# Performance work log

Measured on AMD Instinct MI355X. Metric: run time of the kernel, lower is better.

Reference implementation:

```python
import jax, jax.numpy as jnp
import numpy as np

N = 12000       # nodes (Hi-C bins, max_num_nodes)
F_IN = 16       # number_genomic_annotations
HID = 4 * F_IN  # conv1 out = 64
NCLUST = 100    # n_clust
E = 384000      # edges (avg degree 32)


def setup_inputs() -> dict:
    key = jax.random.key(0)
    ks = jax.random.split(key, 8)
    x = jax.random.normal(ks[0], (N, F_IN), dtype=jnp.float32)
    edge_index = jax.random.randint(ks[1], (2, E), 0, N)
    edge_attr = jax.random.uniform(ks[2], (E,), dtype=jnp.float32)
    s1 = 1.0 / np.sqrt(F_IN)
    W1_rel = jax.random.uniform(ks[3], (HID, F_IN), minval=-s1, maxval=s1, dtype=jnp.float32)
    W1_root = jax.random.uniform(ks[4], (HID, F_IN), minval=-s1, maxval=s1, dtype=jnp.float32)
    b1 = jnp.zeros((HID,), jnp.float32)
    s2 = 1.0 / np.sqrt(HID)
    W2_rel = jax.random.uniform(ks[5], (NCLUST, HID), minval=-s2, maxval=s2, dtype=jnp.float32)
    W2_root = jax.random.uniform(ks[6], (NCLUST, HID), minval=-s2, maxval=s2, dtype=jnp.float32)
    b2 = jnp.zeros((NCLUST,), jnp.float32)
    return dict(x=x, edge_index=edge_index, edge_attr=edge_attr,
                W1_rel=W1_rel, W1_root=W1_root, b1=b1,
                W2_rel=W2_rel, W2_root=W2_root, b2=b2)


def _graph_conv(x, src, dst, ew, W_rel, W_root, b):
    # PyG GraphConv (aggr='add'): out = lin_rel(sum_j e_ji * x_j) + lin_root(x)
    msg = x[src] * ew[:, None]                       # [E, F]
    aggr = jax.ops.segment_sum(msg, dst, num_segments=N)  # [N, F]
    return aggr @ W_rel.T + b + x @ W_root.T


def reference(x, edge_index, edge_attr, W1_rel, W1_root, b1, W2_rel, W2_root, b2):
    src, dst = edge_index[0], edge_index[1]
    h = _graph_conv(x, src, dst, edge_attr, W1_rel, W1_root, b1)
    h = jax.nn.relu(h)  # dropout is identity in eval mode
    s_out = _graph_conv(h, src, dst, edge_attr, W2_rel, W2_root, b2)  # [N, NCLUST]

    # to_dense_adj (duplicate edges summed)
    adj = jnp.zeros((N, N), x.dtype).at[src, dst].add(edge_attr)  # [N, N]

    # dense_mincut_pool with S = x (as in the original forward), k = F_IN
    s_mc = jax.nn.softmax(x, axis=-1)      # [N, F_IN]
    as_ = adj @ s_mc                        # [N, F_IN]
    out_adj = s_mc.T @ as_                  # [F_IN, F_IN]
    mincut_num = jnp.trace(out_adj)
    d_flat = adj.sum(-1)                    # [N] degree
    mincut_den = jnp.einsum('ik,i,ik->', s_mc, d_flat, s_mc)  # trace(S^T D S)
    mc = -(mincut_num / mincut_den)

    ss = s_mc.T @ s_mc                      # [F_IN, F_IN]
    i_k = jnp.eye(F_IN, dtype=ss.dtype)
    o = jnp.linalg.norm(ss / jnp.linalg.norm(ss) - i_k / jnp.linalg.norm(i_k))

    return jax.nn.softmax(s_out, axis=-1), mc, o
```

## Files before the change

kernel.cpp:

```cpp
#include <hip/hip_runtime.h>
#include <math.h>

#define N_NODES 12000
#define F_INN 16
#define HIDD 64
#define NCLUST 100
#define NEDGE 384000
#define NBLK_N 47
#define CAP 96
#define EPT 4
#define NBLK_E 375
#define NBLK_F1 (N_NODES / 4)
#define NBLK_F2 (N_NODES / 8)

#define OFF_COUNT   0
#define OFF_SCAL    12000
#define ZERO_ELEMS  12002
#define OFF_SSPART  12004
#define OFF_NORM2   24036
#define OFF_W2TREL  36036
#define OFF_W2TROOT 42436
#define OFF_SMC     48836
#define OFF_H       240836
#define OFF_SRCW    1008836

__global__ void pre_kernel(const float* __restrict__ x, float* __restrict__ smc,
                           float* __restrict__ norm2, const float* __restrict__ W2_rel,
                           const float* __restrict__ W2_root, float* __restrict__ w2t_rel,
                           float* __restrict__ w2t_root) {
    __shared__ float fl[6400];
    int t = threadIdx.x;
    int b = blockIdx.x;
    if (b < NBLK_N) {
        int i = b * 256 + t;
        if (i >= N_NODES) return;
        const float4* xr = (const float4*)(x + i * 16);
        float4 r0 = xr[0], r1 = xr[1], r2 = xr[2], r3 = xr[3];
        float v[16] = {r0.x, r0.y, r0.z, r0.w, r1.x, r1.y, r1.z, r1.w,
                       r2.x, r2.y, r2.z, r2.w, r3.x, r3.y, r3.z, r3.w};
        float m = v[0];
#pragma unroll
        for (int k = 1; k < 16; ++k) m = fmaxf(m, v[k]);
        float s = 0.f;
#pragma unroll
        for (int k = 0; k < 16; ++k) { v[k] = __expf(v[k] - m); s += v[k]; }
        float inv = 1.f / s;
        float n2 = 0.f;
#pragma unroll
        for (int k = 0; k < 16; ++k) { v[k] *= inv; n2 += v[k] * v[k]; }
        float4* so = (float4*)(smc + i * 16);
        so[0] = make_float4(v[0], v[1], v[2], v[3]);
        so[1] = make_float4(v[4], v[5], v[6], v[7]);
        so[2] = make_float4(v[8], v[9], v[10], v[11]);
        so[3] = make_float4(v[12], v[13], v[14], v[15]);
        norm2[i] = n2;
    } else {
        const float* src = (b == NBLK_N) ? W2_rel : W2_root;
        float* dst = (b == NBLK_N) ? w2t_rel : w2t_root;
        for (int i = t; i < 6400; i += 256) fl[i] = src[i];
        __syncthreads();
        for (int j = t; j < 6400; j += 256) {
            int kk = j / 100, cl = j - kk * 100;
            dst[j] = fl[cl * 64 + kk];
        }
    }
}

__global__ void scatter_kernel(const int* __restrict__ ei, const float* __restrict__ ew,
                               int* __restrict__ count, int2* __restrict__ srcw,
                               const float* __restrict__ smc, float* __restrict__ sspart,
                               const float* __restrict__ norm2, float* __restrict__ scal) {
    __shared__ float shm[4352];
    int t = threadIdx.x;
    int b = blockIdx.x;
    if (b < NBLK_E) {
        int tid = b * 256 + t;
        int e0 = tid * EPT;
        int4 sv = *(const int4*)(ei + e0);
        int4 dv = *(const int4*)(ei + NEDGE + e0);
        float4 wv = *(const float4*)(ew + e0);
        int s[EPT] = {sv.x, sv.y, sv.z, sv.w};
        int d[EPT] = {dv.x, dv.y, dv.z, dv.w};
        float w[EPT] = {wv.x, wv.y, wv.z, wv.w};
        int pos[EPT];
#pragma unroll
        for (int i = 0; i < EPT; ++i) pos[i] = atomicAdd(&count[d[i]], 1);
#pragma unroll
        for (int i = 0; i < EPT; ++i)
            srcw[d[i] * CAP + pos[i]] = make_int2(s[i], __float_as_int(w[i]));
    } else if (b < NBLK_E + NBLK_N) {
        int bb = b - NBLK_E;
        float* rows = shm;
        int n = bb * 256 + t;
        float* rp = rows + t * 17;
        if (n < N_NODES) {
            const float4* sr = (const float4*)(smc + n * 16);
            float4 a0 = sr[0], a1 = sr[1], a2v = sr[2], a3 = sr[3];
            rp[0] = a0.x;  rp[1] = a0.y;  rp[2] = a0.z;  rp[3] = a0.w;
            rp[4] = a1.x;  rp[5] = a1.y;  rp[6] = a1.z;  rp[7] = a1.w;
            rp[8] = a2v.x; rp[9] = a2v.y; rp[10] = a2v.z; rp[11] = a2v.w;
            rp[12] = a3.x; rp[13] = a3.y; rp[14] = a3.z; rp[15] = a3.w;
        } else {
#pragma unroll
            for (int k = 0; k < 16; ++k) rp[k] = 0.f;
        }
        __syncthreads();
        int a = t & 15, bq = t >> 4;
        float accs = 0.f;
#pragma unroll 4
        for (int r = 0; r < 256; ++r)
            accs = fmaf(rows[r * 17 + a], rows[r * 17 + bq], accs);
        sspart[bb * 256 + t] = accs;
    } else {
        int tid = (b - NBLK_E - NBLK_N) * 256 + t;
        int e0 = tid * EPT;
        int4 sv = *(const int4*)(ei + e0);
        int4 dv = *(const int4*)(ei + NEDGE + e0);
        float4 wv = *(const float4*)(ew + e0);
        int s[EPT] = {sv.x, sv.y, sv.z, sv.w};
        int d[EPT] = {dv.x, dv.y, dv.z, dv.w};
        float w[EPT] = {wv.x, wv.y, wv.z, wv.w};
        float np = 0.f, dp = 0.f;
#pragma unroll
        for (int i = 0; i < EPT; ++i) {
            const float4* ps = (const float4*)(smc + s[i] * 16);
            const float4* pd = (const float4*)(smc + d[i] * 16);
            float4 s0 = ps[0], s1 = ps[1], s2 = ps[2], s3 = ps[3];
            float4 d0 = pd[0], d1 = pd[1], d2 = pd[2], d3 = pd[3];
            float dot = s0.x * d0.x + s0.y * d0.y + s0.z * d0.z + s0.w * d0.w +
                        s1.x * d1.x + s1.y * d1.y + s1.z * d1.z + s1.w * d1.w +
                        s2.x * d2.x + s2.y * d2.y + s2.z * d2.z + s2.w * d2.w +
                        s3.x * d3.x + s3.y * d3.y + s3.z * d3.z + s3.w * d3.w;
            np = fmaf(w[i], dot, np);
            dp = fmaf(w[i], norm2[s[i]], dp);
        }
        float* redn = shm;
        float* redd = shm + 256;
        redn[t] = np;
        redd[t] = dp;
        __syncthreads();
        for (int s2 = 128; s2 > 0; s2 >>= 1) {
            if (t < s2) { redn[t] += redn[t + s2]; redd[t] += redd[t + s2]; }
            __syncthreads();
        }
        if (t == 0) {
            atomicAdd(&scal[0], redn[0]);
            atomicAdd(&scal[1], redd[0]);
        }
    }
}

__global__ void fused1_kernel(const float* __restrict__ x, const int2* __restrict__ srcw,
                              const int* __restrict__ count, const float* __restrict__ W1_rel,
                              const float* __restrict__ W1_root, const float* __restrict__ b1,
                              float* __restrict__ h) {
    __shared__ float shm[2304];
    int t = threadIdx.x;
    int b = blockIdx.x;
    float* wrelT  = shm;
    float* wrootT = shm + 1024;
    float* b1s    = shm + 2048;
    float* aggr   = shm + 2112;
    float* xs     = shm + 2176;
    for (int idx = t; idx < 1024; idx += 256) {
        int f = idx >> 4, k = idx & 15;
        wrelT[(k << 6) + f]  = W1_rel[idx];
        wrootT[(k << 6) + f] = W1_root[idx];
    }
    if (t < 64) b1s[t] = b1[t];
    int w = t >> 6, lane = t & 63;
    int j2 = lane >> 2;
    int q  = lane & 3;
    int n = b * 4 + w;
    int len = count[n];
    const int2* bucket = srcw + n * CAP;
    float4 acc4 = make_float4(0.f, 0.f, 0.f, 0.f);
    for (int k = 0; k < len; k += 32) {
        int ia = k + j2, ib = k + 16 + j2;
        int2 pa = bucket[ia];
        int2 pb = bucket[ib];
        if (ia >= len) pa = make_int2(0, 0);
        if (ib >= len) pb = make_int2(0, 0);
        float4 va = *(const float4*)(x + pa.x * 16 + q * 4);
        float4 vb = *(const float4*)(x + pb.x * 16 + q * 4);
        float wa = __int_as_float(pa.y), wb = __int_as_float(pb.y);
        acc4.x = fmaf(va.x, wa, acc4.x); acc4.y = fmaf(va.y, wa, acc4.y);
        acc4.z = fmaf(va.z, wa, acc4.z); acc4.w = fmaf(va.w, wa, acc4.w);
        acc4.x = fmaf(vb.x, wb, acc4.x); acc4.y = fmaf(vb.y, wb, acc4.y);
        acc4.z = fmaf(vb.z, wb, acc4.z); acc4.w = fmaf(vb.w, wb, acc4.w);
    }
    acc4.x += __shfl_xor(acc4.x, 4);  acc4.y += __shfl_xor(acc4.y, 4);
    acc4.z += __shfl_xor(acc4.z, 4);  acc4.w += __shfl_xor(acc4.w, 4);
    acc4.x += __shfl_xor(acc4.x, 8);  acc4.y += __shfl_xor(acc4.y, 8);
    acc4.z += __shfl_xor(acc4.z, 8);  acc4.w += __shfl_xor(acc4.w, 8);
    acc4.x += __shfl_xor(acc4.x, 16); acc4.y += __shfl_xor(acc4.y, 16);
    acc4.z += __shfl_xor(acc4.z, 16); acc4.w += __shfl_xor(acc4.w, 16);
    acc4.x += __shfl_xor(acc4.x, 32); acc4.y += __shfl_xor(acc4.y, 32);
    acc4.z += __shfl_xor(acc4.z, 32); acc4.w += __shfl_xor(acc4.w, 32);
    if (j2 == 0) *(float4*)(aggr + w * 16 + q * 4) = acc4;
    if (lane < 16) xs[w * 16 + lane] = x[n * 16 + lane];
    __syncthreads();
    float o = b1s[lane];
#pragma unroll
    for (int kk = 0; kk < 16; ++kk)
        o = fmaf(aggr[w * 16 + kk], wrelT[(kk << 6) + lane],
                 fmaf(xs[w * 16 + kk], wrootT[(kk << 6) + lane], o));
    h[n * 64 + lane] = fmaxf(o, 0.f);
}

__global__ __launch_bounds__(512) void fused2_finalize_kernel(
    const float* __restrict__ h, const int2* __restrict__ srcw, const int* __restrict__ count,
    const float* __restrict__ w2t_rel, const float* __restrict__ w2t_root,
    const float* __restrict__ b2, float* __restrict__ out, const float* __restrict__ sspart,
    const float* __restrict__ scal) {
    __shared__ float wsrel[6400];
    __shared__ float a2[8][64], hrow[8][64];
    __shared__ float logits[8][104];
    __shared__ float b2s[104];
    int t = threadIdx.x;
    int b = blockIdx.x;
    if (b < NBLK_F2) {
        for (int i = t; i < 6400; i += 512) wsrel[i] = w2t_rel[i];
        if (t < NCLUST) b2s[t] = b2[t];
        int nn = t >> 6;
        int c = t & 63;
        int eslot = c >> 4;
        int q = c & 15;
        int n = b * 8 + nn;
        int len = count[n];
        const int2* bucket = srcw + n * CAP;
        float4 acc4 = make_float4(0.f, 0.f, 0.f, 0.f);
        for (int k = 0; k < len; k += 32) {
            int i0 = k + eslot,      i1 = k + 4 + eslot;
            int i2 = k + 8 + eslot,  i3 = k + 12 + eslot;
            int i4 = k + 16 + eslot, i5 = k + 20 + eslot;
            int i6 = k + 24 + eslot, i7 = k + 28 + eslot;
            int2 pa = bucket[i0]; int2 pb = bucket[i1];
            int2 pc = bucket[i2]; int2 pd = bucket[i3];
            int2 pe = bucket[i4]; int2 pf = bucket[i5];
            int2 pg = bucket[i6]; int2 ph = bucket[i7];
            if (i0 >= len) pa = make_int2(0, 0);
            if (i1 >= len) pb = make_int2(0, 0);
            if (i2 >= len) pc = make_int2(0, 0);
            if (i3 >= len) pd = make_int2(0, 0);
            if (i4 >= len) pe = make_int2(0, 0);
            if (i5 >= len) pf = make_int2(0, 0);
            if (i6 >= len) pg = make_int2(0, 0);
            if (i7 >= len) ph = make_int2(0, 0);
            float4 va = *(const float4*)(h + pa.x * 64 + q * 4);
            float4 vb = *(const float4*)(h + pb.x * 64 + q * 4);
            float4 vc = *(const float4*)(h + pc.x * 64 + q * 4);
            float4 vd = *(const float4*)(h + pd.x * 64 + q * 4);
            float4 ve = *(const float4*)(h + pe.x * 64 + q * 4);
            float4 vf = *(const float4*)(h + pf.x * 64 + q * 4);
            float4 vg = *(const float4*)(h + pg.x * 64 + q * 4);
            float4 vh = *(const float4*)(h + ph.x * 64 + q * 4);
            float wa = __int_as_float(pa.y), wb = __int_as_float(pb.y);
            float wc = __int_as_float(pc.y), wd = __int_as_float(pd.y);
            float we = __int_as_float(pe.y), wf = __int_as_float(pf.y);
            float wg = __int_as_float(pg.y), wh = __int_as_float(ph.y);
            acc4.x = fmaf(va.x, wa, acc4.x); acc4.y = fmaf(va.y, wa, acc4.y);
            acc4.z = fmaf(va.z, wa, acc4.z); acc4.w = fmaf(va.w, wa, acc4.w);
            acc4.x = fmaf(vb.x, wb, acc4.x); acc4.y = fmaf(vb.y, wb, acc4.y);
            acc4.z = fmaf(vb.z, wb, acc4.z); acc4.w = fmaf(vb.w, wb, acc4.w);
            acc4.x = fmaf(vc.x, wc, acc4.x); acc4.y = fmaf(vc.y, wc, acc4.y);
            acc4.z = fmaf(vc.z, wc, acc4.z); acc4.w = fmaf(vc.w, wc, acc4.w);
            acc4.x = fmaf(vd.x, wd, acc4.x); acc4.y = fmaf(vd.y, wd, acc4.y);
            acc4.z = fmaf(vd.z, wd, acc4.z); acc4.w = fmaf(vd.w, wd, acc4.w);
            acc4.x = fmaf(ve.x, we, acc4.x); acc4.y = fmaf(ve.y, we, acc4.y);
            acc4.z = fmaf(ve.z, we, acc4.z); acc4.w = fmaf(ve.w, we, acc4.w);
            acc4.x = fmaf(vf.x, wf, acc4.x); acc4.y = fmaf(vf.y, wf, acc4.y);
            acc4.z = fmaf(vf.z, wf, acc4.z); acc4.w = fmaf(vf.w, wf, acc4.w);
            acc4.x = fmaf(vg.x, wg, acc4.x); acc4.y = fmaf(vg.y, wg, acc4.y);
            acc4.z = fmaf(vg.z, wg, acc4.z); acc4.w = fmaf(vg.w, wg, acc4.w);
            acc4.x = fmaf(vh.x, wh, acc4.x); acc4.y = fmaf(vh.y, wh, acc4.y);
            acc4.z = fmaf(vh.z, wh, acc4.z); acc4.w = fmaf(vh.w, wh, acc4.w);
        }
        acc4.x += __shfl_xor(acc4.x, 16); acc4.y += __shfl_xor(acc4.y, 16);
        acc4.z += __shfl_xor(acc4.z, 16); acc4.w += __shfl_xor(acc4.w, 16);
        acc4.x += __shfl_xor(acc4.x, 32); acc4.y += __shfl_xor(acc4.y, 32);
        acc4.z += __shfl_xor(acc4.z, 32); acc4.w += __shfl_xor(acc4.w, 32);
        if (eslot == 0) *(float4*)(&a2[nn][q * 4]) = acc4;
        hrow[nn][c] = h[n * 64 + c];
        __syncthreads();
        int g = t >> 7, c2 = t & 127;
        if (c2 < NCLUST) {
            int na = 2 * g, nb2 = 2 * g + 1;
            float s0 = b2s[c2], s1 = s0;
#pragma unroll 8
            for (int kk = 0; kk < 64; ++kk) {
                float wr = wsrel[kk * 100 + c2];
                float wo = w2t_root[kk * 100 + c2];
                s0 = fmaf(a2[na][kk], wr, fmaf(hrow[na][kk], wo, s0));
                s1 = fmaf(a2[nb2][kk], wr, fmaf(hrow[nb2][kk], wo, s1));
            }
            logits[na][c2] = s0;
            logits[nb2][c2] = s1;
        }
        __syncthreads();
        float v0 = logits[nn][c];
        float v1 = (c < NCLUST - 64) ? logits[nn][64 + c] : -INFINITY;
        float m = fmaxf(v0, v1);
#pragma unroll
        for (int off = 32; off > 0; off >>= 1) m = fmaxf(m, __shfl_xor(m, off));
        float e0 = __expf(v0 - m);
        float e1 = (c < NCLUST - 64) ? __expf(v1 - m) : 0.f;
        float s = e0 + e1;
#pragma unroll
        for (int off = 32; off > 0; off >>= 1) s += __shfl_xor(s, off);
        float inv = 1.f / s;
        out[n * NCLUST + c] = e0 * inv;
        if (c < NCLUST - 64) out[n * NCLUST + 64 + c] = e1 * inv;
    } else {
        float* red = wsrel;
        float sv = 0.f;
        if (t < 256)
            for (int bb = 0; bb < NBLK_N; ++bb) sv += sspart[bb * 256 + t];
        red[t] = sv * sv;
        __syncthreads();
        for (int s = 256; s > 0; s >>= 1) {
            if (t < s) red[t] += red[t + s];
            __syncthreads();
        }
        float ssnorm = sqrtf(red[0]);
        __syncthreads();
        float diff = (t < 256) ? (sv / ssnorm - ((t % 17 == 0) ? 0.25f : 0.f)) : 0.f;
        red[t] = diff * diff;
        __syncthreads();
        for (int s = 256; s > 0; s >>= 1) {
            if (t < s) red[t] += red[t + s];
            __syncthreads();
        }
        if (t == 0) {
            out[N_NODES * NCLUST + 0] = -(scal[0] / scal[1]);
            out[N_NODES * NCLUST + 1] = sqrtf(red[0]);
        }
    }
}

extern "C" void kernel_launch(void* const* d_in, const int* in_sizes, int n_in,
                              void* d_out, int out_size, void* d_ws, size_t ws_size,
                              hipStream_t stream) {
    const float* x       = (const float*)d_in[0];
    const int*   ei      = (const int*)d_in[1];
    const float* ew      = (const float*)d_in[2];
    const float* W1_rel  = (const float*)d_in[3];
    const float* W1_root = (const float*)d_in[4];
    const float* b1      = (const float*)d_in[5];
    const float* W2_rel  = (const float*)d_in[6];
    const float* W2_root = (const float*)d_in[7];
    const float* b2      = (const float*)d_in[8];
    float* out = (float*)d_out;
    int*   wsi = (int*)d_ws;

    int*   count   = wsi + OFF_COUNT;
    float* scal    = (float*)(wsi + OFF_SCAL);
    float* sspart  = (float*)(wsi + OFF_SSPART);
    float* norm2   = (float*)(wsi + OFF_NORM2);
    float* w2trel  = (float*)(wsi + OFF_W2TREL);
    float* w2troot = (float*)(wsi + OFF_W2TROOT);
    float* smc     = (float*)(wsi + OFF_SMC);
    float* h       = (float*)(wsi + OFF_H);
    int2*  srcw    = (int2*)(wsi + OFF_SRCW);

    hipMemsetAsync(wsi, 0, ZERO_ELEMS * sizeof(int), stream);
    pre_kernel<<<NBLK_N + 2, 256, 0, stream>>>(x, smc, norm2, W2_rel, W2_root, w2trel, w2troot);
    scatter_kernel<<<NBLK_E + NBLK_N + NBLK_E, 256, 0, stream>>>(ei, ew, count, srcw,
                                                                 smc, sspart, norm2, scal);
    fused1_kernel<<<NBLK_F1, 256, 0, stream>>>(x, srcw, count, W1_rel, W1_root, b1, h);
    fused2_finalize_kernel<<<NBLK_F2 + 1, 512, 0, stream>>>(h, srcw, count, w2trel, w2troot,
                                                            b2, out, sspart, scal);
}
```

Measured before the change: 99.37 us.

## Replace global atomic edge scatter with two-pass binned bucketing via shared memory

Edges are first grouped into 188 coarse destination bins of 64 nodes. Each block stages records in shared memory and issues one global atomic per bin, spilling to global when a bin overflows its local slot. A second kernel then builds per-node CSR-like buckets in shared memory for each bin and writes them out coalesced. This replaces per-edge global atomics and scattered writes to count/srcw, at the cost of an extra pass over a bin buffer, fixed capacity limits (BCAP, CAP) that drop edges silently if exceeded, and a large shared-memory footprint that reduces occupancy.

```diff
diff --git a/kernel.cpp b/kernel.cpp
--- a/kernel.cpp
+++ b/kernel.cpp
@@ -13,26 +13,70 @@
 #define NBLK_F1 (N_NODES / 4)
 #define NBLK_F2 (N_NODES / 8)
 
-#define OFF_COUNT   0
-#define OFF_SCAL    12000
-#define ZERO_ELEMS  12002
-#define OFF_SSPART  12004
-#define OFF_NORM2   24036
-#define OFF_W2TREL  36036
-#define OFF_W2TROOT 42436
-#define OFF_SMC     48836
-#define OFF_H       240836
-#define OFF_SRCW    1008836
-
-__global__ void pre_kernel(const float* __restrict__ x, float* __restrict__ smc,
-                           float* __restrict__ norm2, const float* __restrict__ W2_rel,
-                           const float* __restrict__ W2_root, float* __restrict__ w2t_rel,
-                           float* __restrict__ w2t_root) {
-    __shared__ float fl[6400];
+#define NBIN 188
+#define BINW 64
+#define BCAP 2560
+#define STCAP 24
+
+#define OFF_BINCNT  0
+#define OFF_SCAL    188
+#define ZERO_ELEMS  190
+#define OFF_COUNT   192
+#define OFF_SSPART  12192
+#define OFF_NORM2   24224
+#define OFF_W2TREL  36224
+#define OFF_W2TROOT 42624
+#define OFF_SMC     49024
+#define OFF_H       241024
+#define OFF_SRCW    1009024
+#define OFF_BINBUF  3313024
+
+__global__ void binA_kernel(const float* __restrict__ x, const int* __restrict__ ei,
+                            const float* __restrict__ ew, float* __restrict__ smc,
+                            float* __restrict__ norm2, int* __restrict__ bincnt,
+                            int2* __restrict__ binbuf, const float* __restrict__ W2_rel,
+                            const float* __restrict__ W2_root, float* __restrict__ w2t_rel,
+                            float* __restrict__ w2t_root) {
+    __shared__ int shmA[188 + 188 * STCAP * 2];
     int t = threadIdx.x;
     int b = blockIdx.x;
-    if (b < NBLK_N) {
-        int i = b * 256 + t;
+    if (b < NBLK_E) {
+        int* scnt = shmA;
+        int2* sbuf = (int2*)(shmA + 188);
+        for (int i = t; i < 188; i += 256) scnt[i] = 0;
+        __syncthreads();
+        int tid = b * 256 + t;
+        int e0 = tid * EPT;
+        int4 sv = *(const int4*)(ei + e0);
+        int4 dv = *(const int4*)(ei + NEDGE + e0);
+        float4 wv = *(const float4*)(ew + e0);
+        int s[EPT] = {sv.x, sv.y, sv.z, sv.w};
+        int d[EPT] = {dv.x, dv.y, dv.z, dv.w};
+        float w[EPT] = {wv.x, wv.y, wv.z, wv.w};
+#pragma unroll
+        for (int i = 0; i < EPT; ++i) {
+            int bin = d[i] >> 6;
+            int dl = d[i] & 63;
+            int2 rec = make_int2(s[i] | (dl << 16), __float_as_int(w[i]));
+            int pos = atomicAdd(&scnt[bin], 1);
+            if (pos < STCAP) {
+                sbuf[bin * STCAP + pos] = rec;
+            } else {
+                int base = atomicAdd(&bincnt[bin], 1);
+                binbuf[bin * BCAP + base] = rec;
+            }
+        }
+        __syncthreads();
+        if (t < 188) {
+            int k = scnt[t];
+            if (k > STCAP) k = STCAP;
+            if (k > 0) {
+                int base = atomicAdd(&bincnt[t], k);
+                for (int i = 0; i < k; ++i) binbuf[t * BCAP + base + i] = sbuf[t * STCAP + i];
+            }
+        }
+    } else if (b < NBLK_E + NBLK_N) {
+        int i = (b - NBLK_E) * 256 + t;
         if (i >= N_NODES) return;
         const float4* xr = (const float4*)(x + i * 16);
         float4 r0 = xr[0], r1 = xr[1], r2 = xr[2], r3 = xr[3];
@@ -55,8 +99,9 @@
         so[3] = make_float4(v[12], v[13], v[14], v[15]);
         norm2[i] = n2;
     } else {
-        const float* src = (b == NBLK_N) ? W2_rel : W2_root;
-        float* dst = (b == NBLK_N) ? w2t_rel : w2t_root;
+        float* fl = (float*)shmA;
+        const float* src = (b == NBLK_E + NBLK_N) ? W2_rel : W2_root;
+        float* dst = (b == NBLK_E + NBLK_N) ? w2t_rel : w2t_root;
         for (int i = t; i < 6400; i += 256) fl[i] = src[i];
         __syncthreads();
         for (int j = t; j < 6400; j += 256) {
@@ -66,31 +111,39 @@
     }
 }
 
-__global__ void scatter_kernel(const int* __restrict__ ei, const float* __restrict__ ew,
-                               int* __restrict__ count, int2* __restrict__ srcw,
-                               const float* __restrict__ smc, float* __restrict__ sspart,
-                               const float* __restrict__ norm2, float* __restrict__ scal) {
-    __shared__ float shm[4352];
+__global__ void binB_kernel(const int2* __restrict__ binbuf, const int* __restrict__ bincnt,
+                            int* __restrict__ count, int2* __restrict__ srcw,
+                            const float* __restrict__ smc, float* __restrict__ sspart,
+                            const int* __restrict__ ei, const float* __restrict__ ew,
+                            const float* __restrict__ norm2, float* __restrict__ scal) {
+    __shared__ int shmB[64 + 64 * CAP * 2];
     int t = threadIdx.x;
     int b = blockIdx.x;
-    if (b < NBLK_E) {
-        int tid = b * 256 + t;
-        int e0 = tid * EPT;
-        int4 sv = *(const int4*)(ei + e0);
-        int4 dv = *(const int4*)(ei + NEDGE + e0);
-        float4 wv = *(const float4*)(ew + e0);
-        int s[EPT] = {sv.x, sv.y, sv.z, sv.w};
-        int d[EPT] = {dv.x, dv.y, dv.z, dv.w};
-        float w[EPT] = {wv.x, wv.y, wv.z, wv.w};
-        int pos[EPT];
-#pragma unroll
-        for (int i = 0; i < EPT; ++i) pos[i] = atomicAdd(&count[d[i]], 1);
-#pragma unroll
-        for (int i = 0; i < EPT; ++i)
-            srcw[d[i] * CAP + pos[i]] = make_int2(s[i], __float_as_int(w[i]));
-    } else if (b < NBLK_E + NBLK_N) {
-        int bb = b - NBLK_E;
-        float* rows = shm;
+    if (b < NBIN) {
+        int* cnt = shmB;
+        int2* lbuck = (int2*)(shmB + 64);
+        for (int i = t; i < 64; i += 256) cnt[i] = 0;
+        __syncthreads();
+        int nE = bincnt[b];
+        const int2* bp = binbuf + b * BCAP;
+        for (int i = t; i < nE; i += 256) {
+            int2 rec = bp[i];
+            int src = rec.x & 0xFFFF;
+            int dl = rec.x >> 16;
+            int pos = atomicAdd(&cnt[dl], 1);
+            if (pos < CAP) lbuck[dl * CAP + pos] = make_int2(src, rec.y);
+        }
+        __syncthreads();
+        int nbase = b * BINW;
+        int nvalid = N_NODES - nbase;
+        if (nvalid > BINW) nvalid = BINW;
+        if (t < nvalid) count[nbase + t] = cnt[t];
+        int lim = nvalid * CAP;
+        int2* out = srcw + (size_t)nbase * CAP;
+        for (int i = t; i < lim; i += 256) out[i] = lbuck[i];
+    } else if (b < NBIN + NBLK_N) {
+        int bb = b - NBIN;
+        float* rows = (float*)shmB;
         int n = bb * 256 + t;
         float* rp = rows + t * 17;
         if (n < N_NODES) {
@@ -112,7 +165,7 @@
             accs = fmaf(rows[r * 17 + a], rows[r * 17 + bq], accs);
         sspart[bb * 256 + t] = accs;
     } else {
-        int tid = (b - NBLK_E - NBLK_N) * 256 + t;
+        int tid = (b - NBIN - NBLK_N) * 256 + t;
         int e0 = tid * EPT;
         int4 sv = *(const int4*)(ei + e0);
         int4 dv = *(const int4*)(ei + NEDGE + e0);
@@ -134,8 +187,8 @@
             np = fmaf(w[i], dot, np);
             dp = fmaf(w[i], norm2[s[i]], dp);
         }
-        float* redn = shm;
-        float* redd = shm + 256;
+        float* redn = (float*)shmB;
+        float* redd = (float*)shmB + 256;
         redn[t] = np;
         redd[t] = dp;
         __syncthreads();
@@ -353,8 +406,9 @@
     float* out = (float*)d_out;
     int*   wsi = (int*)d_ws;
 
+    int*   bincnt  = wsi + OFF_BINCNT;
+    float* scal    = (float*)(wsi + OFF_SCAL);
     int*   count   = wsi + OFF_COUNT;
-    float* scal    = (float*)(wsi + OFF_SCAL);
     float* sspart  = (float*)(wsi + OFF_SSPART);
     float* norm2   = (float*)(wsi + OFF_NORM2);
     float* w2trel  = (float*)(wsi + OFF_W2TREL);
@@ -362,11 +416,13 @@
     float* smc     = (float*)(wsi + OFF_SMC);
     float* h       = (float*)(wsi + OFF_H);
     int2*  srcw    = (int2*)(wsi + OFF_SRCW);
+    int2*  binbuf  = (int2*)(wsi + OFF_BINBUF);
 
     hipMemsetAsync(wsi, 0, ZERO_ELEMS * sizeof(int), stream);
-    pre_kernel<<<NBLK_N + 2, 256, 0, stream>>>(x, smc, norm2, W2_rel, W2_root, w2trel, w2troot);
-    scatter_kernel<<<NBLK_E + NBLK_N + NBLK_E, 256, 0, stream>>>(ei, ew, count, srcw,
-                                                                 smc, sspart, norm2, scal);
+    binA_kernel<<<NBLK_E + NBLK_N + 2, 256, 0, stream>>>(x, ei, ew, smc, norm2, bincnt, binbuf,
+                                                         W2_rel, W2_root, w2trel, w2troot);
+    binB_kernel<<<NBIN + NBLK_N + NBLK_E, 256, 0, stream>>>(binbuf, bincnt, count, srcw,
+                                                            smc, sspart, ei, ew, norm2, scal);
     fused1_kernel<<<NBLK_F1, 256, 0, stream>>>(x, srcw, count, W1_rel, W1_root, b1, h);
     fused2_finalize_kernel<<<NBLK_F2 + 1, 512, 0, stream>>>(h, srcw, count, w2trel, w2troot,
                                                             b2, out, sspart, scal);
```

Result: faster. 90.45 us (-9.0%).
